# Performance work log

Hardware: AMD Instinct MI355X
Metric: run time of the kernel (lower is better)

Reference implementation:

```python
import jax, jax.numpy as jnp
import numpy as np

NUM_BINS = 40
EPS = 1e-8


def build_zg():
    # z_bin_ctrs[i] = i * pi/2 / 39, zg[i,j] = clamp(cos(|z_i - z_j|), 0, 1)
    z = jnp.arange(NUM_BINS, dtype=jnp.float32) * (np.pi / 2.0 / (NUM_BINS - 1))
    zg = jnp.cos(jnp.abs(z[:, None] - z[None, :]))
    return jnp.clip(zg, 0.0, 1.0)


def setup_inputs() -> dict:
    key = jax.random.key(0)
    k1, k2 = jax.random.split(key)
    batch_label = jax.random.randint(k1, (8192,), 0, NUM_BINS, dtype=jnp.int64 if jax.config.jax_enable_x64 else jnp.int32)
    batch_feat = jax.random.normal(k2, (8192, 512), dtype=jnp.float32)
    return {"batch_label": batch_label, "batch_feat": batch_feat}


def reference(batch_label, batch_feat):
    zg = build_zg()  # [40, 40] constant graph
    # label adjacency: zg gathered at (label_i, label_j) -> [bs, bs]
    lbl_adj = zg[batch_label[:, None], batch_label[None, :]]
    # feature adjacency: cosine-similarity Gram matrix
    # torch cosine_similarity uses denom = max(||x||*||y||, eps)
    norms = jnp.maximum(jnp.linalg.norm(batch_feat, axis=-1, keepdims=True), EPS)
    fn = batch_feat / norms
    feat_adj = fn @ fn.T  # [bs, bs]
    # MSE loss (mean over all bs*bs entries)
    diff = feat_adj - lbl_adj
    return jnp.mean(diff * diff)
```

## Files before the change

### kernel.cpp

```cpp
#include <hip/hip_runtime.h>
#include <hip/hip_bf16.h>


typedef __attribute__((ext_vector_type(8))) short bf16x8;
typedef __attribute__((ext_vector_type(4))) float f32x4;

#define NROW 8192
#define DIM  512
#define NBIN 40
#define NBLK 64
#define NPAIR (NBLK*(NBLK+1)/2)
#define BK 32
#define NT (DIM/BK)
#define TELEM (128*BK)

__device__ __forceinline__ unsigned short f2bf(float x) {
  __hip_bfloat16 h = __float2bfloat16(x);
  union { __hip_bfloat16 h; unsigned short u; } cv;
  cv.h = h;
  return cv.u;
}

__global__ __launch_bounds__(256) void rownorm_kernel(const float* __restrict__ feat,
                                                      __hip_bfloat16* __restrict__ fn) {
  int wid  = threadIdx.x >> 6;
  int lane = threadIdx.x & 63;
  int row  = blockIdx.x * 4 + wid;
  const float4* src = (const float4*)(feat + (size_t)row * DIM);
  float4 a = src[lane];
  float4 b = src[lane + 64];
  float s = a.x*a.x + a.y*a.y + a.z*a.z + a.w*a.w
          + b.x*b.x + b.y*b.y + b.z*b.z + b.w*b.w;
#pragma unroll
  for (int off = 1; off < 64; off <<= 1) s += __shfl_xor(s, off, 64);
  float scale = 1.0f / fmaxf(sqrtf(s), 1e-8f);
  ushort4 o0, o1;
  o0.x = f2bf(a.x * scale); o0.y = f2bf(a.y * scale);
  o0.z = f2bf(a.z * scale); o0.w = f2bf(a.w * scale);
  o1.x = f2bf(b.x * scale); o1.y = f2bf(b.y * scale);
  o1.z = f2bf(b.z * scale); o1.w = f2bf(b.w * scale);
  ushort4* dst = (ushort4*)(fn + (size_t)row * DIM);
  dst[lane]      = o0;
  dst[lane + 64] = o1;
}

__global__ __launch_bounds__(256, 4) void loss_kernel(const __hip_bfloat16* __restrict__ fn,
                                                      const int* __restrict__ label,
                                                      double* __restrict__ partials) {
  __shared__ __hip_bfloat16 Abuf[2][TELEM];
  __shared__ __hip_bfloat16 Bbuf[2][TELEM];
  __shared__ float zd[NBIN];
  __shared__ int   lbl[256];
  __shared__ float wsum[4];

  const int tid  = threadIdx.x;
  const int wid  = tid >> 6;
  const int lane = tid & 63;
  const int wr   = wid >> 1;
  const int wc   = wid & 1;

  const int t0 = (blockIdx.x & 7) * (NPAIR / 8) + (blockIdx.x >> 3);

  int bi = 0;
  while (bi < NBLK - 1 && (bi + 1) * NBLK - ((bi + 1) * bi) / 2 <= t0) bi++;
  const int bj = bi + (t0 - (bi * NBLK - (bi * (bi - 1)) / 2));
  const int i0 = bi * 128;
  const int j0 = bj * 128;

  if (tid < NBIN) {
    float d = (float)tid * (float)(1.5707963267948966 / (NBIN - 1));
    zd[tid] = fminf(fmaxf(cosf(d), 0.0f), 1.0f);
  }
  lbl[tid] = (tid < 128) ? label[i0 + tid] : label[j0 + tid - 128];

  const __hip_bfloat16* srcA[2];
  const __hip_bfloat16* srcB[2];
  int dstOff[2];
#pragma unroll
  for (int q = 0; q < 2; ++q) {
    const int L   = q * 256 + tid;
    const int row = L >> 2;
    const int cg  = (L & 3) ^ ((row >> 1) & 3);
    srcA[q] = fn + (size_t)(i0 + row) * DIM + cg * 8;
    srcB[q] = fn + (size_t)(j0 + row) * DIM + cg * 8;
    dstOff[q] = (q * 256 + wid * 64) * 16;
  }

  auto issueTile = [&](int tt, int bb) {
#pragma unroll
    for (int q = 0; q < 2; ++q)
      __builtin_amdgcn_global_load_lds(
          (const __attribute__((address_space(1))) void*)(srcA[q] + tt * BK),
          (__attribute__((address_space(3))) void*)((char*)&Abuf[bb][0] + dstOff[q]),
          16, 0, 0);
#pragma unroll
    for (int q = 0; q < 2; ++q)
      __builtin_amdgcn_global_load_lds(
          (const __attribute__((address_space(1))) void*)(srcB[q] + tt * BK),
          (__attribute__((address_space(3))) void*)((char*)&Bbuf[bb][0] + dstOff[q]),
          16, 0, 0);
  };

  issueTile(0, 0);
  asm volatile("s_waitcnt vmcnt(0)" ::: "memory");
  __builtin_amdgcn_s_barrier();

  f32x4 acc[4][4] = {};
  const int fr = lane & 15;
  const int fc = lane >> 4;
  const int cx = fc ^ ((fr >> 1) & 3);
  const int arow0 = wr * 64 + fr;
  const int brow0 = wc * 64 + fr;

  for (int t = 0; t < NT; ++t) {
    const int c = t & 1;
    const __hip_bfloat16* Ab = &Abuf[c][0];
    const __hip_bfloat16* Bb = &Bbuf[c][0];

    bf16x8 af[4], bf[4];
#pragma unroll
    for (int m = 0; m < 4; ++m)
      af[m] = *(const bf16x8*)&Ab[(arow0 + m * 16) * BK + cx * 8];
#pragma unroll
    for (int n = 0; n < 4; ++n)
      bf[n] = *(const bf16x8*)&Bb[(brow0 + n * 16) * BK + cx * 8];

    if (t < NT - 1) issueTile(t + 1, c ^ 1);

#pragma unroll
    for (int m = 0; m < 4; ++m)
#pragma unroll
      for (int n = 0; n < 4; ++n)
        acc[m][n] = __builtin_amdgcn_mfma_f32_16x16x32_bf16(af[m], bf[n], acc[m][n], 0, 0, 0);

    if (t < NT - 1) {
      asm volatile("s_waitcnt vmcnt(0)" ::: "memory");
      __builtin_amdgcn_s_barrier();
    }
  }

  const int rb4 = (lane >> 4) * 4;
  int ljv[4];
#pragma unroll
  for (int n = 0; n < 4; ++n) ljv[n] = lbl[128 + wc * 64 + n * 16 + fr];
  float lsum = 0.0f;
#pragma unroll
  for (int m = 0; m < 4; ++m) {
#pragma unroll
    for (int r = 0; r < 4; ++r) {
      const int li = lbl[wr * 64 + m * 16 + rb4 + r];
#pragma unroll
      for (int n = 0; n < 4; ++n) {
        int dd = li - ljv[n]; if (dd < 0) dd = -dd;
        float d = acc[m][n][r] - zd[dd];
        lsum += d * d;
      }
    }
  }
  if (bi != bj) lsum *= 2.0f;

#pragma unroll
  for (int off = 1; off < 64; off <<= 1) lsum += __shfl_xor(lsum, off, 64);
  if (lane == 0) wsum[wid] = lsum;
  __syncthreads();
  if (tid == 0)
    partials[blockIdx.x] = (double)((wsum[0] + wsum[1]) + (wsum[2] + wsum[3]));
}

__global__ __launch_bounds__(256) void finalize_kernel(const double* __restrict__ partials,
                                                       int nblk, float* __restrict__ out) {
  __shared__ double wsh[4];
  int wid = threadIdx.x >> 6, lane = threadIdx.x & 63;
  double s = 0.0;
  for (int i = threadIdx.x; i < nblk; i += 256) s += partials[i];
#pragma unroll
  for (int off = 1; off < 64; off <<= 1) s += __shfl_xor(s, off, 64);
  if (lane == 0) wsh[wid] = s;
  __syncthreads();
  if (threadIdx.x == 0) {
    double tot = wsh[0] + wsh[1] + wsh[2] + wsh[3];
    out[0] = (float)(tot / ((double)NROW * (double)NROW));
  }
}

extern "C" void kernel_launch(void* const* d_in, const int* in_sizes, int n_in,
                              void* d_out, int out_size, void* d_ws, size_t ws_size,
                              hipStream_t stream) {
  const int*   label = (const int*)d_in[0];
  const float* feat  = (const float*)d_in[1];
  float* out = (float*)d_out;

  char* ws = (char*)d_ws;
  __hip_bfloat16* fn = (__hip_bfloat16*)ws;
  double* partials = (double*)(ws + (size_t)NROW * DIM * 2);

  rownorm_kernel<<<NROW / 4, 256, 0, stream>>>(feat, fn);
  loss_kernel<<<NPAIR, 256, 0, stream>>>(fn, label, partials);
  finalize_kernel<<<1, 256, 0, stream>>>(partials, NPAIR, out);
}
```

Measured before the change: 119.5 us.

## Triple-buffer LDS tiles and double-buffer register fragments in Gram loss kernel

Replaces the two-stage LDS pipeline with three stages, keeping two tiles of global-to-LDS loads in flight with partial vmcnt waits. Fragments for the next k-step are read from LDS into a second register set before the current MFMA block runs, so LDS reads overlap matrix math. MFMA sections are wrapped in raised wave priority. LDS use grows to three buffers per operand and the occupancy hint drops from 4 to 3 blocks, which adds register and LDS pressure.

New measurement: 116.1 us. 2.8% less time.

```diff
diff --git a/kernel.cpp b/kernel.cpp
--- a/kernel.cpp
+++ b/kernel.cpp
@@ -44,11 +44,11 @@
   dst[lane + 64] = o1;
 }
 
-__global__ __launch_bounds__(256, 4) void loss_kernel(const __hip_bfloat16* __restrict__ fn,
+__global__ __launch_bounds__(256, 3) void loss_kernel(const __hip_bfloat16* __restrict__ fn,
                                                       const int* __restrict__ label,
                                                       double* __restrict__ partials) {
-  __shared__ __hip_bfloat16 Abuf[2][TELEM];
-  __shared__ __hip_bfloat16 Bbuf[2][TELEM];
+  __shared__ __hip_bfloat16 Abuf[3][TELEM];
+  __shared__ __hip_bfloat16 Bbuf[3][TELEM];
   __shared__ float zd[NBIN];
   __shared__ int   lbl[256];
   __shared__ float wsum[4];
@@ -72,6 +72,7 @@
     zd[tid] = fminf(fmaxf(cosf(d), 0.0f), 1.0f);
   }
   lbl[tid] = (tid < 128) ? label[i0 + tid] : label[j0 + tid - 128];
+  asm volatile("s_waitcnt vmcnt(0)" ::: "memory");
 
   const __hip_bfloat16* srcA[2];
   const __hip_bfloat16* srcB[2];
@@ -101,43 +102,63 @@
           16, 0, 0);
   };
 
-  issueTile(0, 0);
-  asm volatile("s_waitcnt vmcnt(0)" ::: "memory");
-  __builtin_amdgcn_s_barrier();
-
-  f32x4 acc[4][4] = {};
   const int fr = lane & 15;
   const int fc = lane >> 4;
   const int cx = fc ^ ((fr >> 1) & 3);
   const int arow0 = wr * 64 + fr;
   const int brow0 = wc * 64 + fr;
 
-  for (int t = 0; t < NT; ++t) {
-    const int c = t & 1;
-    const __hip_bfloat16* Ab = &Abuf[c][0];
-    const __hip_bfloat16* Bb = &Bbuf[c][0];
-
-    bf16x8 af[4], bf[4];
-#pragma unroll
-    for (int m = 0; m < 4; ++m)
-      af[m] = *(const bf16x8*)&Ab[(arow0 + m * 16) * BK + cx * 8];
-#pragma unroll
-    for (int n = 0; n < 4; ++n)
-      bf[n] = *(const bf16x8*)&Bb[(brow0 + n * 16) * BK + cx * 8];
-
-    if (t < NT - 1) issueTile(t + 1, c ^ 1);
-
-#pragma unroll
-    for (int m = 0; m < 4; ++m)
-#pragma unroll
-      for (int n = 0; n < 4; ++n)
-        acc[m][n] = __builtin_amdgcn_mfma_f32_16x16x32_bf16(af[m], bf[n], acc[m][n], 0, 0, 0);
-
-    if (t < NT - 1) {
-      asm volatile("s_waitcnt vmcnt(0)" ::: "memory");
-      __builtin_amdgcn_s_barrier();
-    }
-  }
+  issueTile(0, 0); issueTile(1, 1); issueTile(2, 2);
+  asm volatile("s_waitcnt vmcnt(4)" ::: "memory");
+  __builtin_amdgcn_s_barrier();
+
+  f32x4 acc[4][4] = {};
+  bf16x8 afX[4], bfX[4], afY[4], bfY[4];
+
+#pragma unroll
+  for (int m = 0; m < 4; ++m)
+    afX[m] = *(const bf16x8*)&Abuf[0][(arow0 + m * 16) * BK + cx * 8];
+#pragma unroll
+  for (int n = 0; n < 4; ++n)
+    bfX[n] = *(const bf16x8*)&Bbuf[0][(brow0 + n * 16) * BK + cx * 8];
+  asm volatile("s_waitcnt lgkmcnt(0)" ::: "memory");
+  __builtin_amdgcn_s_barrier();
+
+#define BODY(T, AC, BC, AN, BN)                                                  \
+  {                                                                              \
+    const int t_ = (T);                                                          \
+    if (t_ + 3 < NT) issueTile(t_ + 3, t_ % 3);                                  \
+    if (t_ + 1 < NT) {                                                           \
+      const int b1 = (t_ + 1) % 3;                                               \
+      _Pragma("unroll")                                                          \
+      for (int m = 0; m < 4; ++m)                                                \
+        AN[m] = *(const bf16x8*)&Abuf[b1][(arow0 + m * 16) * BK + cx * 8];       \
+      _Pragma("unroll")                                                          \
+      for (int n = 0; n < 4; ++n)                                                \
+        BN[n] = *(const bf16x8*)&Bbuf[b1][(brow0 + n * 16) * BK + cx * 8];       \
+    }                                                                            \
+    __builtin_amdgcn_s_setprio(1);                                               \
+    _Pragma("unroll")                                                            \
+    for (int m = 0; m < 4; ++m)                                                  \
+      _Pragma("unroll")                                                          \
+      for (int n = 0; n < 4; ++n)                                                \
+        acc[m][n] = __builtin_amdgcn_mfma_f32_16x16x32_bf16(AC[m], BC[n],        \
+                                                            acc[m][n], 0, 0, 0); \
+    __builtin_amdgcn_s_setprio(0);                                               \
+    if (t_ < NT - 1) {                                                           \
+      if (t_ < NT - 3) asm volatile("s_waitcnt vmcnt(4)" ::: "memory");          \
+      else             asm volatile("s_waitcnt vmcnt(0)" ::: "memory");          \
+          \
+      asm volatile("s_waitcnt lgkmcnt(0)" ::: "memory");                         \
+      __builtin_amdgcn_s_barrier();                                              \
+    }                                                                            \
+  }
+
+  for (int t = 0; t < NT; t += 2) {
+    BODY(t,     afX, bfX, afY, bfY);
+    BODY(t + 1, afY, bfY, afX, bfX);
+  }
+#undef BODY
 
   const int rb4 = (lane >> 4) * 4;
   int ljv[4];
```
